# Optimization experiments

Hardware: AMD Instinct MI355X
Metric: run time of the kernel (lower is better)

The kernel has to match this reference:

```python
import jax, jax.numpy as jnp
import numpy as np

D_MODEL = 1024
N_DIM = 64      # per-head dim; scores scaled by 1/sqrt(n_dim)
N_HEADS = 16
SEQ = 4096
LN_EPS = 1e-5


def setup_inputs() -> dict:
    key = jax.random.key(0)
    ks = jax.random.split(key, 12)
    hd = N_HEADS * N_DIM  # == D_MODEL (required by residual add)
    s = 0.02
    return {
        "embed_word_vec": jax.random.normal(ks[0], (SEQ, D_MODEL), dtype=jnp.float32),
        "attn_mask": jax.random.uniform(ks[1], (SEQ, SEQ)) < 0.1,  # True = masked out
        "wq": jax.random.normal(ks[2], (D_MODEL, hd), dtype=jnp.float32) * s,
        "bq": jnp.zeros((hd,), dtype=jnp.float32),
        "wk": jax.random.normal(ks[3], (D_MODEL, hd), dtype=jnp.float32) * s,
        "bk": jnp.zeros((hd,), dtype=jnp.float32),
        "wv": jax.random.normal(ks[4], (D_MODEL, hd), dtype=jnp.float32) * s,
        "bv": jnp.zeros((hd,), dtype=jnp.float32),
        "wo": jax.random.normal(ks[5], (hd, D_MODEL), dtype=jnp.float32) * s,
        "bo": jnp.zeros((D_MODEL,), dtype=jnp.float32),
        "gamma": jnp.ones((D_MODEL,), dtype=jnp.float32),
        "beta": jnp.zeros((D_MODEL,), dtype=jnp.float32),
    }


def reference(embed_word_vec, attn_mask, wq, bq, wk, bk, wv, bv, wo, bo, gamma, beta):
    x = embed_word_vec                      # [S, d_model]
    q = x @ wq + bq                         # [S, H*D]
    k = x @ wk + bk
    v = x @ wv + bv
    scores = (q @ k.T) / jnp.sqrt(jnp.asarray(N_DIM, dtype=q.dtype))  # [S, S]
    scores = jnp.where(attn_mask, jnp.asarray(-jnp.inf, dtype=scores.dtype), scores)
    attention = jax.nn.softmax(scores, axis=-1)                       # [S, S]
    context = attention @ v + x             # AV + residual, [S, d_model]
    h = context @ wo + bo                   # out projection
    # LayerNorm over last dim
    mu = jnp.mean(h, axis=-1, keepdims=True)
    var = jnp.mean(jnp.square(h - mu), axis=-1, keepdims=True)
    output = (h - mu) * jax.lax.rsqrt(var + LN_EPS) * gamma + beta
    return (output, attention)
```

## Files before the change

kernel.cpp:

```cpp
#include <hip/hip_runtime.h>
#include <hip/hip_bf16.h>
#include <stdint.h>

#define SEQ 4096
#define DM  1024

typedef __attribute__((ext_vector_type(8))) short bf16x8;
typedef __attribute__((ext_vector_type(4))) float f32x4;

template <int V> struct Int { static constexpr int v = V; };

__device__ __forceinline__ short f2bf(float f) {
  union { float f; unsigned int i; } x; x.f = f;
  unsigned int r = x.i + 0x7FFFu + ((x.i >> 16) & 1u);
  return (short)(r >> 16);
}
__device__ __forceinline__ float bf2f(short s) {
  union { unsigned int i; float f; } u;
  u.i = ((unsigned int)(unsigned short)s) << 16;
  return u.f;
}

__device__ __forceinline__ void gload16(const short* g, short* l) {
  __builtin_amdgcn_global_load_lds(
      (const __attribute__((address_space(1))) unsigned int*)g,
      (__attribute__((address_space(3))) unsigned int*)l, 16, 0, 0);
}

__device__ __forceinline__ float wave_max(float v) {
#pragma unroll
  for (int o = 32; o; o >>= 1) v = fmaxf(v, __shfl_xor(v, o));
  return v;
}
__device__ __forceinline__ float wave_sum(float v) {
#pragma unroll
  for (int o = 32; o; o >>= 1) v += __shfl_xor(v, o);
  return v;
}

#define BARRIER() do { asm volatile("" ::: "memory"); \
  __builtin_amdgcn_s_barrier(); asm volatile("" ::: "memory"); } while (0)
#define MF(a, b, c) __builtin_amdgcn_mfma_f32_16x16x32_bf16(a, b, c, 0, 0, 0)

template <int EPI>
__global__ __launch_bounds__(512, 2) void gemm8(
    const short* __restrict__ A, const short* __restrict__ B,
    short* __restrict__ C, const float* __restrict__ bias,
    int Ksplit, int lda, int ldb, int ldc,
    float scale, int ntm, int ntn, long csplit) {
  __shared__ short lds[2][4][8192];
  const int tid = threadIdx.x;
  const int lane = tid & 63;
  const int wid = tid >> 6;
  const int wr = wid >> 2;
  const int wc = wid & 3;
  const int bid = blockIdx.x, nwg = gridDim.x;
  int wg = (bid & 7) * (nwg >> 3) + (bid >> 3);
  const int tpg = ntm * ntn;
  const int split = wg / tpg;
  wg -= split * tpg;
  const int m0 = (wg / ntn) * 256;
  const int n0 = (wg % ntn) * 256;
  const short* Ab = A + (long)split * Ksplit;
  const short* Bb = B + (long)split * Ksplit;
  short* Co = C + (long)split * csplit;

  const int o0 = tid * 16;
  const int oo = o0 ^ (((o0 >> 7) & 7) << 4);
  const int sr0 = oo >> 7;
  const int sc0 = (oo & 127) >> 1;

  auto stA = [&](int buf, int h, int kt) {
    const short* g = Ab + (long)(m0 + h * 128 + sr0) * lda + kt * 64 + sc0;
    short* l = &lds[buf][h][0] + wid * 512;
    gload16(g, l);
    gload16(g + (long)64 * lda, l + 4096);
  };
  auto stB = [&](int buf, int h, int kt) {
    const short* g = Bb + (long)(n0 + h * 128 + sr0) * ldb + kt * 64 + sc0;
    short* l = &lds[buf][2 + h][0] + wid * 512;
    gload16(g, l);
    gload16(g + (long)64 * ldb, l + 4096);
  };

  const int ll = lane & 15, lh = lane >> 4;
  auto ldaf = [&](int buf, int c, int mm, int kk) {
    const int r = c * 32 + mm * 16 + ll;
    const int off = (r * 64 + kk * 32 + lh * 8) ^ ((r & 7) << 3);
    return *(const bf16x8*)(&lds[buf][wr][0] + off);
  };
  auto ldbf = [&](int buf, int n, int kk) {
    const int r = (wc & 1) * 64 + n * 16 + ll;
    const int off = (r * 64 + kk * 32 + lh * 8) ^ ((r & 7) << 3);
    return *(const bf16x8*)(&lds[buf][2 + (wc >> 1)][0] + off);
  };

  f32x4 acc[8][4];
#pragma unroll
  for (int i = 0; i < 8; i++)
#pragma unroll
    for (int j = 0; j < 4; j++) acc[i][j] = (f32x4){0.f, 0.f, 0.f, 0.f};
  bf16x8 Bf[4][2];

  const int NT = Ksplit >> 6;
  stB(0, 0, 0); stB(0, 1, 0);
  stA(0, 0, 0); stA(0, 1, 0);
  stB(1, 0, 1); stB(1, 1, 1);
  asm volatile("s_waitcnt vmcnt(4)" ::: "memory");
  BARRIER();

  auto phase = [&](auto BUF, auto CC, auto LB, auto&& stg, auto&& tail) {
    constexpr int buf = decltype(BUF)::v;
    constexpr int c = decltype(CC)::v;
    if constexpr (decltype(LB)::v != 0) {
#pragma unroll
      for (int n = 0; n < 4; n++) {
        Bf[n][0] = ldbf(buf, n, 0);
        Bf[n][1] = ldbf(buf, n, 1);
      }
    }
    bf16x8 a00 = ldaf(buf, c, 0, 0), a01 = ldaf(buf, c, 0, 1);
    bf16x8 a10 = ldaf(buf, c, 1, 0), a11 = ldaf(buf, c, 1, 1);
    stg();
    BARRIER();
    __builtin_amdgcn_s_setprio(1);
#pragma unroll
    for (int n = 0; n < 4; n++) {
      acc[2 * c][n] = MF(a00, Bf[n][0], acc[2 * c][n]);
      acc[2 * c][n] = MF(a01, Bf[n][1], acc[2 * c][n]);
      acc[2 * c + 1][n] = MF(a10, Bf[n][0], acc[2 * c + 1][n]);
      acc[2 * c + 1][n] = MF(a11, Bf[n][1], acc[2 * c + 1][n]);
    }
    __builtin_amdgcn_s_setprio(0);
    tail();
    BARRIER();
  };

  for (int t = 0; t < NT; t += 2) {
    const bool nl = (t + 2 < NT);
    phase(Int<0>{}, Int<0>{}, Int<1>{}, [&] { stA(1, 0, t + 1); }, [] {});
    phase(Int<0>{}, Int<1>{}, Int<0>{}, [&] { stA(1, 1, t + 1); }, [] {});
    phase(Int<0>{}, Int<2>{}, Int<0>{}, [&] { if (nl) stB(0, 0, t + 2); },
          [] {});
    phase(Int<0>{}, Int<3>{}, Int<0>{}, [&] { if (nl) stB(0, 1, t + 2); },
          [&] {
            if (nl) { asm volatile("s_waitcnt vmcnt(4)" ::: "memory"); }
            else    { asm volatile("s_waitcnt vmcnt(0)" ::: "memory"); }
          });
    phase(Int<1>{}, Int<0>{}, Int<1>{}, [&] { if (nl) stA(0, 0, t + 2); },
          [] {});
    phase(Int<1>{}, Int<1>{}, Int<0>{}, [&] { if (nl) stA(0, 1, t + 2); },
          [] {});
    phase(Int<1>{}, Int<2>{}, Int<0>{}, [&] { if (nl) stB(1, 0, t + 3); },
          [] {});
    phase(Int<1>{}, Int<3>{}, Int<0>{}, [&] { if (nl) stB(1, 1, t + 3); },
          [&] {
            if (nl) { asm volatile("s_waitcnt vmcnt(4)" ::: "memory"); }
            else    { asm volatile("s_waitcnt vmcnt(0)" ::: "memory"); }
          });
  }

  const int rb = m0 + wr * 128 + lh * 4;
  const int cb0 = n0 + wc * 64 + ll;
#pragma unroll
  for (int mi = 0; mi < 8; mi++) {
#pragma unroll
    for (int n = 0; n < 4; n++) {
      const int col = cb0 + n * 16;
      float bv = 0.f;
      if (EPI == 1) bv = bias[col];
#pragma unroll
      for (int r = 0; r < 4; r++) {
        const int row = rb + mi * 16 + r;
        const long off = (long)row * ldc + col;
        float v = acc[mi][n][r];
        if (EPI == 1) v += bv;
        if (EPI == 2) v *= scale;
        Co[off] = f2bf(v);
      }
    }
  }
}


__global__ __launch_bounds__(256) void cvt_f32_to_bf16(
    const float* __restrict__ in, short* __restrict__ out, int n4) {
  int i = blockIdx.x * 256 + threadIdx.x;
  if (i < n4) {
    float4 f = ((const float4*)in)[i];
    short4 o;
    o.x = f2bf(f.x); o.y = f2bf(f.y); o.z = f2bf(f.z); o.w = f2bf(f.w);
    ((short4*)out)[i] = o;
  }
}

__global__ void transpose_w(const float* __restrict__ in,
                            short* __restrict__ out, int R, int C) {
  __shared__ float tile[32][33];
  const int bx = blockIdx.x * 32;
  const int by = blockIdx.y * 32;
  const int tx = threadIdx.x, ty = threadIdx.y;
#pragma unroll
  for (int i = 0; i < 32; i += 8)
    tile[ty + i][tx] = in[(long)(by + ty + i) * C + bx + tx];
  __syncthreads();
#pragma unroll
  for (int i = 0; i < 32; i += 8)
    out[(long)(bx + ty + i) * R + by + tx] = f2bf(tile[tx][ty + i]);
}

__global__ void transpose_b_ld(const short* __restrict__ in,
                               short* __restrict__ out, int R, int C, int ldin) {
  __shared__ short tile[32][33];
  const int bx = blockIdx.x * 32;
  const int by = blockIdx.y * 32;
  const int tx = threadIdx.x, ty = threadIdx.y;
#pragma unroll
  for (int i = 0; i < 32; i += 8)
    tile[ty + i][tx] = in[(long)(by + ty + i) * ldin + bx + tx];
  __syncthreads();
#pragma unroll
  for (int i = 0; i < 32; i += 8)
    out[(long)(bx + ty + i) * R + by + tx] = tile[tx][ty + i];
}

__global__ __launch_bounds__(256) void softmax_rows(const short* __restrict__ Sb,
                                                    const int* __restrict__ mask,
                                                    short* __restrict__ Pb) {
  const long row = blockIdx.x;
  const bf16x8* src = (const bf16x8*)(Sb + row * SEQ);
  const int* mrow = mask + row * (long)SEQ;
  bf16x8* dst = (bf16x8*)(Pb + row * SEQ);
  const int tid = threadIdx.x;
  const int wid = tid >> 6, lane = tid & 63;
  bf16x8 a = src[tid], b = src[tid + 256];
  int4 ma0 = *(const int4*)(mrow + tid * 8);
  int4 ma1 = *(const int4*)(mrow + tid * 8 + 4);
  int4 mb0 = *(const int4*)(mrow + 2048 + tid * 8);
  int4 mb1 = *(const int4*)(mrow + 2048 + tid * 8 + 4);
  float v[16];
#pragma unroll
  for (int j = 0; j < 8; j++) { v[j] = bf2f(a[j]); v[8 + j] = bf2f(b[j]); }
  const int* mm0 = (const int*)&ma0;
  const int* mm1 = (const int*)&ma1;
  const int* mm2 = (const int*)&mb0;
  const int* mm3 = (const int*)&mb1;
#pragma unroll
  for (int j = 0; j < 4; j++) {
    if (mm0[j]) v[j] = -INFINITY;
    if (mm1[j]) v[4 + j] = -INFINITY;
    if (mm2[j]) v[8 + j] = -INFINITY;
    if (mm3[j]) v[12 + j] = -INFINITY;
  }
  float mx = -INFINITY;
#pragma unroll
  for (int j = 0; j < 16; j++) mx = fmaxf(mx, v[j]);
  mx = wave_max(mx);
  __shared__ float red[4];
  if (lane == 0) red[wid] = mx;
  __syncthreads();
  mx = fmaxf(fmaxf(red[0], red[1]), fmaxf(red[2], red[3]));
  float sum = 0.f;
#pragma unroll
  for (int j = 0; j < 16; j++) {
    v[j] = __expf(v[j] - mx);
    sum += v[j];
  }
  sum = wave_sum(sum);
  __shared__ float red2[4];
  if (lane == 0) red2[wid] = sum;
  __syncthreads();
  sum = red2[0] + red2[1] + red2[2] + red2[3];
  const float inv = 1.0f / sum;
  bf16x8 o0, o1;
#pragma unroll
  for (int j = 0; j < 8; j++) {
    o0[j] = f2bf(v[j] * inv);
    o1[j] = f2bf(v[8 + j] * inv);
  }
  dst[tid] = o0;
  dst[tid + 256] = o1;
}

__global__ __launch_bounds__(256) void expand_bf16_f32(
    const short* __restrict__ in, float* __restrict__ out) {
  long i = (long)blockIdx.x * 256 + threadIdx.x;
  bf16x8 a = ((const bf16x8*)in)[i];
  float4 lo, hi;
  lo.x = bf2f(a[0]); lo.y = bf2f(a[1]); lo.z = bf2f(a[2]); lo.w = bf2f(a[3]);
  hi.x = bf2f(a[4]); hi.y = bf2f(a[5]); hi.z = bf2f(a[6]); hi.w = bf2f(a[7]);
  ((float4*)out)[2 * i] = lo;
  ((float4*)out)[2 * i + 1] = hi;
}

__global__ __launch_bounds__(256) void reduce_ctx4(
    const short* __restrict__ p, const float* __restrict__ x,
    short* __restrict__ cb) {
  const long i = (long)blockIdx.x * 256 + threadIdx.x;
  bf16x8 a = ((const bf16x8*)p)[i];
  bf16x8 b = ((const bf16x8*)(p + 4194304))[i];
  bf16x8 c = ((const bf16x8*)(p + 8388608))[i];
  bf16x8 d = ((const bf16x8*)(p + 12582912))[i];
  float4 x0 = ((const float4*)x)[2 * i];
  float4 x1 = ((const float4*)x)[2 * i + 1];
  float xs[8] = {x0.x, x0.y, x0.z, x0.w, x1.x, x1.y, x1.z, x1.w};
  bf16x8 o;
#pragma unroll
  for (int j = 0; j < 8; j++)
    o[j] = f2bf(bf2f(a[j]) + bf2f(b[j]) + bf2f(c[j]) + bf2f(d[j]) + xs[j]);
  ((bf16x8*)cb)[i] = o;
}

__global__ __launch_bounds__(256) void ln4(
    const short* __restrict__ ph, const float* __restrict__ bo,
    const float* __restrict__ gamma, const float* __restrict__ beta,
    float* __restrict__ out) {
  const long row = blockIdx.x;
  const int tid = threadIdx.x;
  const int wid = tid >> 6, lane = tid & 63;
  const long base = row * DM + tid * 4;
  short4 p0 = *(const short4*)(ph + base);
  short4 p1 = *(const short4*)(ph + 4194304 + base);
  short4 p2 = *(const short4*)(ph + 8388608 + base);
  short4 p3 = *(const short4*)(ph + 12582912 + base);
  float4 bb = *(const float4*)(bo + tid * 4);
  float v[4];
  v[0] = bf2f(p0.x) + bf2f(p1.x) + bf2f(p2.x) + bf2f(p3.x) + bb.x;
  v[1] = bf2f(p0.y) + bf2f(p1.y) + bf2f(p2.y) + bf2f(p3.y) + bb.y;
  v[2] = bf2f(p0.z) + bf2f(p1.z) + bf2f(p2.z) + bf2f(p3.z) + bb.z;
  v[3] = bf2f(p0.w) + bf2f(p1.w) + bf2f(p2.w) + bf2f(p3.w) + bb.w;
  float s = v[0] + v[1] + v[2] + v[3];
  s = wave_sum(s);
  __shared__ float red[4];
  if (lane == 0) red[wid] = s;
  __syncthreads();
  const float mu = (red[0] + red[1] + red[2] + red[3]) * (1.f / DM);
  float var = 0.f;
#pragma unroll
  for (int j = 0; j < 4; j++) {
    float d = v[j] - mu;
    var += d * d;
  }
  var = wave_sum(var);
  __shared__ float red2[4];
  if (lane == 0) red2[wid] = var;
  __syncthreads();
  var = (red2[0] + red2[1] + red2[2] + red2[3]) * (1.f / DM);
  const float inv = rsqrtf(var + 1e-5f);
  float4 g = *(const float4*)(gamma + tid * 4);
  float4 be = *(const float4*)(beta + tid * 4);
  float4 o;
  o.x = (v[0] - mu) * inv * g.x + be.x;
  o.y = (v[1] - mu) * inv * g.y + be.y;
  o.z = (v[2] - mu) * inv * g.z + be.z;
  o.w = (v[3] - mu) * inv * g.w + be.w;
  *(float4*)(out + base) = o;
}

extern "C" void kernel_launch(void* const* d_in, const int* in_sizes, int n_in,
                              void* d_out, int out_size, void* d_ws,
                              size_t ws_size, hipStream_t stream) {
  const float* x    = (const float*)d_in[0];
  const int* mask   = (const int*)d_in[1];
  const float* wq   = (const float*)d_in[2];
  const float* bq   = (const float*)d_in[3];
  const float* wk   = (const float*)d_in[4];
  const float* bk   = (const float*)d_in[5];
  const float* wv   = (const float*)d_in[6];
  const float* bv   = (const float*)d_in[7];
  const float* wo   = (const float*)d_in[8];
  const float* bo   = (const float*)d_in[9];
  const float* gamma = (const float*)d_in[10];
  const float* beta  = (const float*)d_in[11];

  float* out  = (float*)d_out;
  float* attn = out + 4194304;
  short* Sb   = (short*)attn;
  short* pav  = (short*)attn;
  short* ph   = (short*)(attn + 8388608);
  short* cbuf = (short*)out;

  char* w = (char*)d_ws;
  short* wqkvT = (short*)(w + 0);
  short* woT   = (short*)(w + 6291456);
  short* xb    = (short*)(w + 8388608);
  short* qkv   = (short*)(w + 16777216);
  short* attnb = (short*)(w + 8388608);
  short* vT    = (short*)(w + 41943040);
  float* bqkv  = (float*)(w + 50331648);

  cvt_f32_to_bf16<<<4096, 256, 0, stream>>>(x, xb, 1048576);
  dim3 tb(32, 8);
  transpose_w<<<dim3(32, 32), tb, 0, stream>>>(wq, wqkvT, 1024, 1024);
  transpose_w<<<dim3(32, 32), tb, 0, stream>>>(wk, wqkvT + 1048576, 1024, 1024);
  transpose_w<<<dim3(32, 32), tb, 0, stream>>>(wv, wqkvT + 2097152, 1024, 1024);
  transpose_w<<<dim3(32, 32), tb, 0, stream>>>(wo, woT, 1024, 1024);
  hipMemcpyAsync(bqkv, bq, 4096, hipMemcpyDeviceToDevice, stream);
  hipMemcpyAsync(bqkv + 1024, bk, 4096, hipMemcpyDeviceToDevice, stream);
  hipMemcpyAsync(bqkv + 2048, bv, 4096, hipMemcpyDeviceToDevice, stream);

  gemm8<1><<<192, 512, 0, stream>>>(xb, wqkvT, qkv, bqkv,
                                    1024, 1024, 1024, 3072, 1.f, 16, 12, 0);

  transpose_b_ld<<<dim3(32, 128), tb, 0, stream>>>(qkv + 2048, vT, 4096, 1024, 3072);

  gemm8<2><<<256, 512, 0, stream>>>(qkv, qkv + 1024, Sb, nullptr,
                                    1024, 3072, 3072, 4096, 0.125f, 16, 16, 0);

  softmax_rows<<<SEQ, 256, 0, stream>>>(Sb, mask, attnb);

  gemm8<0><<<256, 512, 0, stream>>>(attnb, vT, pav, nullptr,
                                    1024, 4096, 4096, 1024, 1.f, 16, 4,
                                    4194304L);

  reduce_ctx4<<<2048, 256, 0, stream>>>(pav, x, cbuf);

  gemm8<0><<<256, 512, 0, stream>>>(cbuf, woT, ph, nullptr,
                                    256, 1024, 1024, 1024, 1.f, 16, 4,
                                    4194304L);

  ln4<<<SEQ, 256, 0, stream>>>(ph, bo, gamma, beta, out);

  expand_bf16_f32<<<8192, 256, 0, stream>>>(attnb, attn);
}
```

Baseline: 214.0 us.

## Batch weight transposes and bias concat into single launches, regroup GEMM prefetch stages

Merges the four weight transpose kernels into one launch indexed by blockIdx.z, and replaces three device-to-device bias memcpys with a single small concat kernel, cutting launch and memcpy overhead. The GEMM main loop also now issues both halves of each A/B tile prefetch in one phase, leaving the third and fourth phases of each half free of loads. This front-loads global-to-LDS traffic, giving loads more time to land before the wait, but the bursts can contend with MFMA work in the early phases.

Result: faster. 206.9 us (-3.3%).

```diff
diff --git a/kernel.cpp b/kernel.cpp
--- a/kernel.cpp
+++ b/kernel.cpp
@@ -138,26 +138,24 @@
 
   for (int t = 0; t < NT; t += 2) {
     const bool nl = (t + 2 < NT);
-    phase(Int<0>{}, Int<0>{}, Int<1>{}, [&] { stA(1, 0, t + 1); }, [] {});
-    phase(Int<0>{}, Int<1>{}, Int<0>{}, [&] { stA(1, 1, t + 1); }, [] {});
-    phase(Int<0>{}, Int<2>{}, Int<0>{}, [&] { if (nl) stB(0, 0, t + 2); },
-          [] {});
-    phase(Int<0>{}, Int<3>{}, Int<0>{}, [&] { if (nl) stB(0, 1, t + 2); },
-          [&] {
-            if (nl) { asm volatile("s_waitcnt vmcnt(4)" ::: "memory"); }
-            else    { asm volatile("s_waitcnt vmcnt(0)" ::: "memory"); }
-          });
-    phase(Int<1>{}, Int<0>{}, Int<1>{}, [&] { if (nl) stA(0, 0, t + 2); },
-          [] {});
-    phase(Int<1>{}, Int<1>{}, Int<0>{}, [&] { if (nl) stA(0, 1, t + 2); },
-          [] {});
-    phase(Int<1>{}, Int<2>{}, Int<0>{}, [&] { if (nl) stB(1, 0, t + 3); },
-          [] {});
-    phase(Int<1>{}, Int<3>{}, Int<0>{}, [&] { if (nl) stB(1, 1, t + 3); },
-          [&] {
-            if (nl) { asm volatile("s_waitcnt vmcnt(4)" ::: "memory"); }
-            else    { asm volatile("s_waitcnt vmcnt(0)" ::: "memory"); }
-          });
+    phase(Int<0>{}, Int<0>{}, Int<1>{},
+          [&] { stA(1, 0, t + 1); stA(1, 1, t + 1); }, [] {});
+    phase(Int<0>{}, Int<1>{}, Int<0>{},
+          [&] { if (nl) { stB(0, 0, t + 2); stB(0, 1, t + 2); } }, [] {});
+    phase(Int<0>{}, Int<2>{}, Int<0>{}, [] {}, [] {});
+    phase(Int<0>{}, Int<3>{}, Int<0>{}, [] {}, [&] {
+      if (nl) { asm volatile("s_waitcnt vmcnt(4)" ::: "memory"); }
+      else    { asm volatile("s_waitcnt vmcnt(0)" ::: "memory"); }
+    });
+    phase(Int<1>{}, Int<0>{}, Int<1>{},
+          [&] { if (nl) { stA(0, 0, t + 2); stA(0, 1, t + 2); } }, [] {});
+    phase(Int<1>{}, Int<1>{}, Int<0>{},
+          [&] { if (nl) { stB(1, 0, t + 3); stB(1, 1, t + 3); } }, [] {});
+    phase(Int<1>{}, Int<2>{}, Int<0>{}, [] {}, [] {});
+    phase(Int<1>{}, Int<3>{}, Int<0>{}, [] {}, [&] {
+      if (nl) { asm volatile("s_waitcnt vmcnt(4)" ::: "memory"); }
+      else    { asm volatile("s_waitcnt vmcnt(0)" ::: "memory"); }
+    });
   }
 
   const int rb = m0 + wr * 128 + lh * 4;
@@ -194,19 +192,26 @@
   }
 }
 
-__global__ void transpose_w(const float* __restrict__ in,
-                            short* __restrict__ out, int R, int C) {
+__global__ void transpose_w4(const float* __restrict__ s0,
+                             const float* __restrict__ s1,
+                             const float* __restrict__ s2,
+                             const float* __restrict__ s3,
+                             short* __restrict__ d0, short* __restrict__ d1,
+                             short* __restrict__ d2, short* __restrict__ d3) {
+  const int z = blockIdx.z;
+  const float* in = z == 0 ? s0 : z == 1 ? s1 : z == 2 ? s2 : s3;
+  short* out = z == 0 ? d0 : z == 1 ? d1 : z == 2 ? d2 : d3;
   __shared__ float tile[32][33];
   const int bx = blockIdx.x * 32;
   const int by = blockIdx.y * 32;
   const int tx = threadIdx.x, ty = threadIdx.y;
 #pragma unroll
   for (int i = 0; i < 32; i += 8)
-    tile[ty + i][tx] = in[(long)(by + ty + i) * C + bx + tx];
+    tile[ty + i][tx] = in[(long)(by + ty + i) * 1024 + bx + tx];
   __syncthreads();
 #pragma unroll
   for (int i = 0; i < 32; i += 8)
-    out[(long)(bx + ty + i) * R + by + tx] = f2bf(tile[tx][ty + i]);
+    out[(long)(bx + ty + i) * 1024 + by + tx] = f2bf(tile[tx][ty + i]);
 }
 
 __global__ void transpose_b_ld(const short* __restrict__ in,
@@ -222,6 +227,14 @@
 #pragma unroll
   for (int i = 0; i < 32; i += 8)
     out[(long)(bx + ty + i) * R + by + tx] = tile[tx][ty + i];
+}
+
+__global__ __launch_bounds__(256) void concat_bias(
+    const float* __restrict__ bq, const float* __restrict__ bk,
+    const float* __restrict__ bv, float* __restrict__ o) {
+  int i = blockIdx.x * 256 + threadIdx.x;
+  float v = (i < 1024) ? bq[i] : (i < 2048 ? bk[i - 1024] : bv[i - 2048]);
+  o[i] = v;
 }
 
 __global__ __launch_bounds__(256) void softmax_rows(const short* __restrict__ Sb,
@@ -390,19 +403,15 @@
   float* bqkv  = (float*)(w + 50331648);
 
   cvt_f32_to_bf16<<<4096, 256, 0, stream>>>(x, xb, 1048576);
-  dim3 tb(32, 8);
-  transpose_w<<<dim3(32, 32), tb, 0, stream>>>(wq, wqkvT, 1024, 1024);
-  transpose_w<<<dim3(32, 32), tb, 0, stream>>>(wk, wqkvT + 1048576, 1024, 1024);
-  transpose_w<<<dim3(32, 32), tb, 0, stream>>>(wv, wqkvT + 2097152, 1024, 1024);
-  transpose_w<<<dim3(32, 32), tb, 0, stream>>>(wo, woT, 1024, 1024);
-  hipMemcpyAsync(bqkv, bq, 4096, hipMemcpyDeviceToDevice, stream);
-  hipMemcpyAsync(bqkv + 1024, bk, 4096, hipMemcpyDeviceToDevice, stream);
-  hipMemcpyAsync(bqkv + 2048, bv, 4096, hipMemcpyDeviceToDevice, stream);
+  transpose_w4<<<dim3(32, 32, 4), dim3(32, 8), 0, stream>>>(
+      wq, wk, wv, wo, wqkvT, wqkvT + 1048576, wqkvT + 2097152, woT);
+  concat_bias<<<12, 256, 0, stream>>>(bq, bk, bv, bqkv);
 
   gemm8<1><<<192, 512, 0, stream>>>(xb, wqkvT, qkv, bqkv,
                                     1024, 1024, 1024, 3072, 1.f, 16, 12, 0);
 
-  transpose_b_ld<<<dim3(32, 128), tb, 0, stream>>>(qkv + 2048, vT, 4096, 1024, 3072);
+  transpose_b_ld<<<dim3(32, 128), dim3(32, 8), 0, stream>>>(qkv + 2048, vT,
+                                                            4096, 1024, 3072);
 
   gemm8<2><<<256, 512, 0, stream>>>(qkv, qkv + 1024, Sb, nullptr,
                                     1024, 3072, 3072, 4096, 0.125f, 16, 16, 0);
```
